# Kernel tuning notes

Hardware: AMD Instinct MI355X
Metric: run time of the kernel (lower is better)

## Reference

```python
import jax, jax.numpy as jnp
import numpy as np
import math

D_MODEL = 2048
N_HEADS = 16
D_K = D_MODEL // N_HEADS  # 128
B = 2
L = 2048


def _rope_cos_sin(seq_len, d_k, dtype):
    inv_freq = 1.0 / (10000.0 ** (jnp.arange(0, d_k, 2, dtype=jnp.float32) / d_k))
    t = jnp.arange(seq_len, dtype=jnp.float32)
    freqs = jnp.outer(t, inv_freq)  # [L, d_k//2]
    return jnp.cos(freqs).astype(dtype), jnp.sin(freqs).astype(dtype)


def _apply_rope(x, cos, sin):
    # x: [B, H, L, d_k]; cos/sin: [L, d_k//2] broadcast over B,H
    half = x.shape[-1] // 2
    x1, x2 = x[..., :half], x[..., half:]
    c = cos[None, None, :, :]
    s = sin[None, None, :, :]
    return jnp.concatenate([x1 * c - x2 * s, x1 * s + x2 * c], axis=-1)


def setup_inputs() -> dict:
    key = jax.random.key(0)
    ks = jax.random.split(key, 8)
    scale = 1.0 / math.sqrt(D_MODEL)
    query = jax.random.normal(ks[0], (B, L, D_MODEL), dtype=jnp.float32)
    k_in = jax.random.normal(ks[1], (B, L, D_MODEL), dtype=jnp.float32)
    v_in = jax.random.normal(ks[2], (B, L, D_MODEL), dtype=jnp.float32)
    w_q = jax.random.normal(ks[3], (D_MODEL, D_MODEL), dtype=jnp.float32) * scale
    w_k = jax.random.normal(ks[4], (D_MODEL, D_MODEL), dtype=jnp.float32) * scale
    w_v = jax.random.normal(ks[5], (D_MODEL, D_MODEL), dtype=jnp.float32) * scale
    w_o = jax.random.normal(ks[6], (D_MODEL, D_MODEL), dtype=jnp.float32) * scale
    mask = jnp.tril(jnp.ones((L, L), dtype=bool))[None, None, :, :]
    return {"query": query, "key": k_in, "value": v_in, "mask": mask,
            "w_q": w_q, "w_k": w_k, "w_v": w_v, "w_o": w_o}


def reference(query, key, value, mask, w_q, w_k, w_v, w_o):
    Bq, Lq, D = query.shape
    Lk = key.shape[1]
    # Linear (no bias): y = x @ W.T ; split heads -> [B, H, L, d_k]
    def proj(x, w, length):
        y = jnp.einsum('bld,ed->ble', x, w)
        return y.reshape(x.shape[0], length, N_HEADS, D_K).transpose(0, 2, 1, 3)
    Q = proj(query, w_q, Lq)
    K = proj(key, w_k, Lk)
    V = proj(value, w_v, Lk)
    cos_q, sin_q = _rope_cos_sin(Lq, D_K, query.dtype)
    cos_k, sin_k = _rope_cos_sin(Lk, D_K, key.dtype)
    Q = _apply_rope(Q, cos_q, sin_q)
    K = _apply_rope(K, cos_k, sin_k)
    scores = jnp.einsum('bhqd,bhkd->bhqk', Q, K) / math.sqrt(D_K)
    neg = jnp.finfo(scores.dtype).min
    scores = jnp.where(mask, scores, neg)
    attn = jax.nn.softmax(scores, axis=-1)
    out = jnp.einsum('bhqk,bhkd->bhqd', attn, V)
    out = out.transpose(0, 2, 1, 3).reshape(Bq, Lq, D)
    return jnp.einsum('bld,ed->ble', out, w_o)
```

## Files before the change

### kernel.cpp

```cpp
#include <hip/hip_runtime.h>
#include <stdint.h>

#define L_SEQ 2048
#define DMODEL 2048
#define NHEADS 16
#define DK 128
#define BATCH 2
#define MROWS (BATCH*L_SEQ)

typedef float f32x4 __attribute__((ext_vector_type(4)));
typedef short s16x8 __attribute__((ext_vector_type(8)));
typedef unsigned short u16;
typedef unsigned int u32;

__device__ __forceinline__ u16 f2bf(float f){
  u32 u = __builtin_bit_cast(u32, f);
  u += 0x7fffu + ((u >> 16) & 1u);
  return (u16)(u >> 16);
}
__device__ __forceinline__ float bf2f(u16 h){
  u32 u = ((u32)h) << 16;
  return __builtin_bit_cast(float, u);
}
__device__ __forceinline__ void gload_lds16(const void* g, void* l){
  __builtin_amdgcn_global_load_lds((const __attribute__((address_space(1))) void*)g,
                                   (__attribute__((address_space(3))) void*)l, 16, 0, 0);
}

__global__ void k_cvt_all(const float* __restrict__ s0, const float* __restrict__ s1,
                          const float* __restrict__ s2, const float* __restrict__ s3,
                          const float* __restrict__ s4, const float* __restrict__ s5,
                          const float* __restrict__ s6,
                          u16* __restrict__ d0, u16* __restrict__ d1, u16* __restrict__ d2,
                          u16* __restrict__ d3, u16* __restrict__ d4, u16* __restrict__ d5,
                          u16* __restrict__ d6){
  const int XC = MROWS*DMODEL/8;
  const int WC = DMODEL*DMODEL/8;
  const int total = 3*XC + 4*WC;
  int stride = gridDim.x * blockDim.x;
  for (int i = blockIdx.x*blockDim.x + threadIdx.x; i < total; i += stride){
    const float* s; u16* d; int j;
    if (i < XC)        { s=s0; d=d0; j=i; }
    else if (i < 2*XC) { s=s1; d=d1; j=i-XC; }
    else if (i < 3*XC) { s=s2; d=d2; j=i-2*XC; }
    else {
      int k2 = i - 3*XC; int wi = k2 / WC; j = k2 - wi*WC;
      s = wi==0?s3 : wi==1?s4 : wi==2?s5 : s6;
      d = wi==0?d3 : wi==1?d4 : wi==2?d5 : d6;
    }
    const f32x4* sp = (const f32x4*)s + (size_t)j*2;
    f32x4 a = sp[0], b = sp[1];
    s16x8 o;
    o[0]=(short)f2bf(a[0]); o[1]=(short)f2bf(a[1]); o[2]=(short)f2bf(a[2]); o[3]=(short)f2bf(a[3]);
    o[4]=(short)f2bf(b[0]); o[5]=(short)f2bf(b[1]); o[6]=(short)f2bf(b[2]); o[7]=(short)f2bf(b[3]);
    ((s16x8*)d)[j] = o;
  }
}

__global__ void k_tab(float* __restrict__ ct, float* __restrict__ st){
  int idx = blockIdx.x*blockDim.x + threadIdx.x;
  int l = idx >> 6, i = idx & 63;
  float e = (float)i * (1.0f/64.0f);
  float inv = 1.0f / powf(10000.0f, e);
  float fr = (float)l * inv;
  ct[idx] = cosf(fr);
  st[idx] = sinf(fr);
}

__global__ void k_rope2(u16* __restrict__ xq, u16* __restrict__ xk,
                        const float* __restrict__ ct, const float* __restrict__ st){
  int t0 = blockIdx.x*blockDim.x + threadIdx.x;
  u16* x = (t0 & (1<<19)) ? xk : xq;
  int t = t0 & ((1<<19)-1);
  int i8  = (t & 7) * 8;
  int h   = (t >> 3) & 15;
  int row = t >> 7;
  int l   = row & (L_SEQ-1);
  u16* p = x + (size_t)row*DMODEL + h*DK;
  s16x8 a  = *(s16x8*)(p + i8);
  s16x8 bq = *(s16x8*)(p + 64 + i8);
  const float* cp = ct + l*64 + i8;
  const float* sp = st + l*64 + i8;
  f32x4 c0 = *(const f32x4*)cp, c1 = *(const f32x4*)(cp+4);
  f32x4 s0 = *(const f32x4*)sp, s1 = *(const f32x4*)(sp+4);
  float cc[8] = {c0[0],c0[1],c0[2],c0[3],c1[0],c1[1],c1[2],c1[3]};
  float ss[8] = {s0[0],s0[1],s0[2],s0[3],s1[0],s1[1],s1[2],s1[3]};
  s16x8 y1, y2;
  #pragma unroll
  for (int e=0;e<8;e++){
    float x1 = bf2f((u16)a[e]), x2 = bf2f((u16)bq[e]);
    y1[e] = (short)f2bf(x1*cc[e] - x2*ss[e]);
    y2[e] = (short)f2bf(x1*ss[e] + x2*cc[e]);
  }
  *(s16x8*)(p + i8)      = y1;
  *(s16x8*)(p + 64 + i8) = y2;
}

__global__ __launch_bounds__(256)
void k_gemm3(const u16* __restrict__ A0, const u16* __restrict__ A1, const u16* __restrict__ A2,
             const u16* __restrict__ B0, const u16* __restrict__ B1, const u16* __restrict__ B2,
             u16* __restrict__ C0, u16* __restrict__ C1, u16* __restrict__ C2){
  __shared__ u16 As[128*64];
  __shared__ u16 Bs[128*64];
  const int z = blockIdx.z;
  const u16* __restrict__ A  = z==0?A0 : z==1?A1 : A2;
  const u16* __restrict__ Bw = z==0?B0 : z==1?B1 : B2;
  u16* __restrict__ Cb       = z==0?C0 : z==1?C1 : C2;
  const int tid = threadIdx.x, w = tid>>6, l = tid&63;
  const int lg = l>>4, lr = l&15;
  const int lin = (int)blockIdx.y*16 + (int)blockIdx.x;
  const int lin2 = (lin&7)*64 + (lin>>3);
  const int bm = (lin2>>4)*128, bn = (lin2&15)*128;
  const int K = DMODEL, N = DMODEL;
  f32x4 acc[4][4];
  #pragma unroll
  for (int i=0;i<4;i++)
    #pragma unroll
    for (int j=0;j<4;j++) acc[i][j] = (f32x4){0.f,0.f,0.f,0.f};

  const int chunkbase = w*64 + l;
  const int wm = (w>>1)*64, wn = (w&1)*64;

  for (int k0 = 0; k0 < K; k0 += 64){
    __syncthreads();
    #pragma unroll
    for (int i=0;i<4;i++){
      int chunk = i*256 + chunkbase;
      int row = chunk >> 3;
      int cbs = ((chunk&7)<<4) ^ ((row&7)<<4);
      const u16* ga = A  + (size_t)(bm+row)*K + k0 + (cbs>>1);
      const u16* gb = Bw + (size_t)(bn+row)*K + k0 + (cbs>>1);
      gload_lds16(ga, (void*)&As[(i*256 + w*64)*8]);
      gload_lds16(gb, (void*)&Bs[(i*256 + w*64)*8]);
    }
    __syncthreads();
    #pragma unroll
    for (int kc=0; kc<2; kc++){
      s16x8 af[4], bfr[4];
      #pragma unroll
      for (int mi=0; mi<4; mi++){
        int row = wm + mi*16 + lr;
        int off = row*128 + ((kc*64 + lg*16) ^ ((row&7)<<4));
        af[mi] = *(const s16x8*)((const char*)As + off);
      }
      #pragma unroll
      for (int ni=0; ni<4; ni++){
        int row = wn + ni*16 + lr;
        int off = row*128 + ((kc*64 + lg*16) ^ ((row&7)<<4));
        bfr[ni] = *(const s16x8*)((const char*)Bs + off);
      }
      #pragma unroll
      for (int mi=0; mi<4; mi++)
        #pragma unroll
        for (int ni=0; ni<4; ni++)
          acc[mi][ni] = __builtin_amdgcn_mfma_f32_16x16x32_bf16(af[mi], bfr[ni], acc[mi][ni], 0,0,0);
    }
  }
  #pragma unroll
  for (int mi=0; mi<4; mi++)
    #pragma unroll
    for (int ni=0; ni<4; ni++)
      #pragma unroll
      for (int r=0; r<4; r++){
        int row = bm + wm + mi*16 + (lg<<2) + r;
        int col = bn + wn + ni*16 + lr;
        Cb[(size_t)row*N + col] = f2bf(acc[mi][ni][r]);
      }
}

__global__ __launch_bounds__(256)
void k_gemm(const u16* __restrict__ A, const u16* __restrict__ Bw,
            float* __restrict__ Cf){
  __shared__ u16 As[128*64];
  __shared__ u16 Bs[128*64];
  const int tid = threadIdx.x, w = tid>>6, l = tid&63;
  const int lg = l>>4, lr = l&15;
  const int lin = (int)blockIdx.y*16 + (int)blockIdx.x;
  const int lin2 = (lin&7)*64 + (lin>>3);
  const int bm = (lin2>>4)*128, bn = (lin2&15)*128;
  const int K = DMODEL, N = DMODEL;
  f32x4 acc[4][4];
  #pragma unroll
  for (int i=0;i<4;i++)
    #pragma unroll
    for (int j=0;j<4;j++) acc[i][j] = (f32x4){0.f,0.f,0.f,0.f};

  const int chunkbase = w*64 + l;
  const int wm = (w>>1)*64, wn = (w&1)*64;

  for (int k0 = 0; k0 < K; k0 += 64){
    __syncthreads();
    #pragma unroll
    for (int i=0;i<4;i++){
      int chunk = i*256 + chunkbase;
      int row = chunk >> 3;
      int cbs = ((chunk&7)<<4) ^ ((row&7)<<4);
      const u16* ga = A  + (size_t)(bm+row)*K + k0 + (cbs>>1);
      const u16* gb = Bw + (size_t)(bn+row)*K + k0 + (cbs>>1);
      gload_lds16(ga, (void*)&As[(i*256 + w*64)*8]);
      gload_lds16(gb, (void*)&Bs[(i*256 + w*64)*8]);
    }
    __syncthreads();
    #pragma unroll
    for (int kc=0; kc<2; kc++){
      s16x8 af[4], bfr[4];
      #pragma unroll
      for (int mi=0; mi<4; mi++){
        int row = wm + mi*16 + lr;
        int off = row*128 + ((kc*64 + lg*16) ^ ((row&7)<<4));
        af[mi] = *(const s16x8*)((const char*)As + off);
      }
      #pragma unroll
      for (int ni=0; ni<4; ni++){
        int row = wn + ni*16 + lr;
        int off = row*128 + ((kc*64 + lg*16) ^ ((row&7)<<4));
        bfr[ni] = *(const s16x8*)((const char*)Bs + off);
      }
      #pragma unroll
      for (int mi=0; mi<4; mi++)
        #pragma unroll
        for (int ni=0; ni<4; ni++)
          acc[mi][ni] = __builtin_amdgcn_mfma_f32_16x16x32_bf16(af[mi], bfr[ni], acc[mi][ni], 0,0,0);
    }
  }
  #pragma unroll
  for (int mi=0; mi<4; mi++)
    #pragma unroll
    for (int ni=0; ni<4; ni++)
      #pragma unroll
      for (int r=0; r<4; r++){
        int row = bm + wm + mi*16 + (lg<<2) + r;
        int col = bn + wn + ni*16 + lr;
        Cf[(size_t)row*N + col] = acc[mi][ni][r];
      }
}

__global__ __launch_bounds__(256)
void k_attn(const u16* __restrict__ Qp, const u16* __restrict__ Kp,
            const u16* __restrict__ Vp, u16* __restrict__ AO){
  __shared__ u16 Ks[2][64*128];
  __shared__ u16 Vs[128*64];
  __shared__ u16 Ps[4][16*72];
  const int tid = threadIdx.x, w = tid>>6, l = tid&63;
  const int lg = l>>4, lr = l&15;
  const int lin = (int)blockIdx.y * (int)gridDim.x + (int)blockIdx.x;
  const int xcd = lin & 7, s8 = lin >> 3;
  const int bh  = xcd*4 + (s8 >> 4);
  const int qtp = s8 & 15;
  const int b = bh>>4, h = bh&15;
  const size_t kvbase = (size_t)(b*L_SEQ)*DMODEL + h*DK;
  const float scale = 0.08838834764831845f;

  u32 vv[2][8];
  s16x8 ones;
  #pragma unroll
  for (int e=0;e<8;e++) ones[e] = (short)0x3F80;

  auto issueK = [&](int j, int buf){
    #pragma unroll
    for (int i=0;i<4;i++){
      int chunk = i*256 + w*64 + l;
      int row = chunk >> 4;
      int cb = ((chunk&15)<<4) ^ ((row&7)<<4);
      const u16* src = Kp + kvbase + (size_t)(j*64 + row)*DMODEL + (cb>>1);
      gload_lds16(src, (void*)&Ks[buf][(i*256 + w*64)*8]);
    }
  };
  auto issueV = [&](int j){
    #pragma unroll
    for (int it=0; it<2; it++){
      int task = it*256 + tid;
      int dp = task & 63, kb = task >> 6;
      const u16* vsrc = Vp + kvbase + (size_t)(j*64 + kb*8)*DMODEL + dp*2;
      #pragma unroll
      for (int e=0;e<8;e++) vv[it][e] = *(const u32*)(vsrc + (size_t)e*DMODEL);
    }
  };
  auto writeV = [&](){
    #pragma unroll
    for (int it=0; it<2; it++){
      int task = it*256 + tid;
      int dp = task & 63, kb = task >> 6;
      int d0 = dp*2;
      s16x8 lo, hi;
      #pragma unroll
      for (int e=0;e<8;e++){ lo[e] = (short)(vv[it][e] & 0xffffu); hi[e] = (short)(vv[it][e] >> 16); }
      int g = ((d0>>1)&7)<<4;
      *(s16x8*)((char*)&Vs[0] + d0*128     + ((kb*16) ^ g)) = lo;
      *(s16x8*)((char*)&Vs[0] + (d0+1)*128 + ((kb*16) ^ g)) = hi;
    }
  };

  for (int half=0; half<2; half++){
    const int qt = half==0 ? qtp : 31-qtp;
    if (half) __syncthreads();

    s16x8 qf[4];
    {
      const u16* qptr = Qp + (size_t)(b*L_SEQ + qt*64 + w*16 + lr)*DMODEL + h*DK + lg*8;
      #pragma unroll
      for (int kc=0; kc<4; kc++) qf[kc] = *(const s16x8*)(qptr + kc*32);
    }
    f32x4 o[9];
    #pragma unroll
    for (int dt=0; dt<9; dt++) o[dt] = (f32x4){0.f,0.f,0.f,0.f};
    float mrow[4] = {-1e30f,-1e30f,-1e30f,-1e30f};

    issueK(0, 0);
    issueV(0);

    for (int j=0; j<=qt; j++){
      const int cur = j & 1;
      asm volatile("s_waitcnt vmcnt(16)" ::: "memory");
      __builtin_amdgcn_sched_barrier(0);
      __builtin_amdgcn_s_barrier();
      __builtin_amdgcn_sched_barrier(0);
      if (j < qt) issueK(j+1, cur^1);

      f32x4 st4[4];
      __builtin_amdgcn_s_setprio(1);
      #pragma unroll
      for (int ni=0; ni<4; ni++){
        f32x4 a = (f32x4){0.f,0.f,0.f,0.f};
        #pragma unroll
        for (int kc=0; kc<4; kc++){
          int row = ni*16 + lr;
          int off = row*256 + ((kc*64 + lg*16) ^ ((row&7)<<4));
          s16x8 kf = *(const s16x8*)((const char*)&Ks[cur][0] + off);
          a = __builtin_amdgcn_mfma_f32_16x16x32_bf16(qf[kc], kf, a, 0,0,0);
        }
        st4[ni] = a;
      }
      __builtin_amdgcn_s_setprio(0);

      float sv[4][4];
      float lanemax = -1e30f;
      const bool diag = (j == qt);
      #pragma unroll
      for (int r=0;r<4;r++){
        #pragma unroll
        for (int ni=0;ni<4;ni++){
          float x = st4[ni][r]*scale;
          if (diag){
            int kg = ni*16 + lr;
            int qg = w*16 + lg*4 + r;
            if (kg > qg) x = -1e30f;
          }
          sv[ni][r] = x;
          lanemax = fmaxf(lanemax, x);
        }
      }
      float mmin = fminf(fminf(mrow[0],mrow[1]), fminf(mrow[2],mrow[3]));
      if (!__all(lanemax <= mmin + 8.0f)){
        #pragma unroll
        for (int r=0;r<4;r++){
          float tm = fmaxf(fmaxf(sv[0][r],sv[1][r]), fmaxf(sv[2][r],sv[3][r]));
          #pragma unroll
          for (int msk=1; msk<16; msk<<=1) tm = fmaxf(tm, __shfl_xor(tm, msk, 64));
          float mn = fmaxf(mrow[r], tm);
          float al = __expf(mrow[r]-mn);
          mrow[r] = mn;
          #pragma unroll
          for (int dt=0;dt<9;dt++) o[dt][r] *= al;
        }
      }
      #pragma unroll
      for (int r=0;r<4;r++){
        #pragma unroll
        for (int ni=0;ni<4;ni++){
          float p = __expf(sv[ni][r]-mrow[r]);
          Ps[w][(lg*4 + r)*72 + ni*16 + lr] = f2bf(p);
        }
      }
      s16x8 pa[2];
      #pragma unroll
      for (int kc=0;kc<2;kc++) pa[kc] = *(const s16x8*)(&Ps[w][lr*72 + kc*32 + lg*8]);

      if (j < qt){ asm volatile("s_waitcnt vmcnt(4)" ::: "memory"); }
      else       { asm volatile("s_waitcnt vmcnt(0)" ::: "memory"); }
      __builtin_amdgcn_sched_barrier(0);
      writeV();
      if (j < qt) issueV(j+1);
      asm volatile("s_waitcnt lgkmcnt(0)" ::: "memory");
      __builtin_amdgcn_sched_barrier(0);
      __builtin_amdgcn_s_barrier();
      __builtin_amdgcn_sched_barrier(0);

      __builtin_amdgcn_s_setprio(1);
      #pragma unroll
      for (int dt=0;dt<8;dt++){
        #pragma unroll
        for (int kc=0;kc<2;kc++){
          int d = dt*16 + lr;
          int off = d*128 + ((kc*64 + lg*16) ^ (((d>>1)&7)<<4));
          s16x8 vf = *(const s16x8*)((const char*)&Vs[0] + off);
          o[dt] = __builtin_amdgcn_mfma_f32_16x16x32_bf16(pa[kc], vf, o[dt], 0,0,0);
        }
      }
      o[8] = __builtin_amdgcn_mfma_f32_16x16x32_bf16(pa[0], ones, o[8], 0,0,0);
      o[8] = __builtin_amdgcn_mfma_f32_16x16x32_bf16(pa[1], ones, o[8], 0,0,0);
      __builtin_amdgcn_s_setprio(0);
    }

    #pragma unroll
    for (int r=0;r<4;r++){
      float inv = 1.0f / o[8][r];
      size_t rowg = (size_t)(b*L_SEQ + qt*64 + w*16 + lg*4 + r);
      #pragma unroll
      for (int dt=0;dt<8;dt++)
        AO[rowg*DMODEL + h*DK + dt*16 + lr] = f2bf(o[dt][r]*inv);
    }
  }
}

extern "C" void kernel_launch(void* const* d_in, const int* in_sizes, int n_in,
                              void* d_out, int out_size, void* d_ws, size_t ws_size,
                              hipStream_t stream){
  const float* q  = (const float*)d_in[0];
  const float* k  = (const float*)d_in[1];
  const float* v  = (const float*)d_in[2];
  const float* wq = (const float*)d_in[4];
  const float* wk = (const float*)d_in[5];
  const float* wv = (const float*)d_in[6];
  const float* wo = (const float*)d_in[7];
  (void)in_sizes; (void)n_in; (void)out_size; (void)ws_size;

  const size_t MD = (size_t)MROWS*DMODEL;
  const size_t DD = (size_t)DMODEL*DMODEL;
  char* ws = (char*)d_ws;
  size_t off = 0;
  auto alloc = [&](size_t bytes)->void*{ void* p = ws + off; off += (bytes + 255) & ~(size_t)255; return p; };
  u16* Xq = (u16*)alloc(MD*2);
  u16* Xk = (u16*)alloc(MD*2);
  u16* Xv = (u16*)alloc(MD*2);
  u16* Wq = (u16*)alloc(DD*2);
  u16* Wk = (u16*)alloc(DD*2);
  u16* Wv = (u16*)alloc(DD*2);
  u16* Wo = (u16*)alloc(DD*2);
  u16* Qp = (u16*)alloc(MD*2);
  u16* Kp = (u16*)alloc(MD*2);
  u16* Vp = (u16*)alloc(MD*2);
  float* ct = (float*)alloc((size_t)L_SEQ*64*4);
  float* st = (float*)alloc((size_t)L_SEQ*64*4);
  u16* AO = Xq;

  k_cvt_all<<<2048,256,0,stream>>>(q, k, v, wq, wk, wv, wo,
                                   Xq, Xk, Xv, Wq, Wk, Wv, Wo);
  k_tab<<<512,256,0,stream>>>(ct, st);

  k_gemm3<<<dim3(16,32,3),256,0,stream>>>(Xq, Xk, Xv, Wq, Wk, Wv, Qp, Kp, Vp);
  k_rope2<<<4096,256,0,stream>>>(Qp, Kp, ct, st);
  k_attn<<<dim3(16,32),256,0,stream>>>(Qp, Kp, Vp, AO);
  k_gemm<<<dim3(16,32),256,0,stream>>>(AO, Wo, (float*)d_out);
}
```

Before: 275.0 us.

## Double-buffer GEMM LDS tiles with 256x128 blocks of 512 threads

Both projection GEMM kernels switch to 256x128 output tiles computed by 8 waves, with double-buffered LDS. The next K-tile's global-to-LDS loads are issued before the current tile's MFMAs, using explicit vmcnt waits and barriers, and MFMA sections get raised wave priority. This aims to hide global load latency behind compute and reuse the B tile across a taller M tile, at the cost of more LDS (96KB per block) and fewer blocks in flight.

New measurement: 301.7 us. 1.1x slower.

```diff
diff --git a/kernel.cpp b/kernel.cpp
--- a/kernel.cpp
+++ b/kernel.cpp
@@ -96,12 +96,12 @@
   *(s16x8*)(p + 64 + i8) = y2;
 }
 
-__global__ __launch_bounds__(256)
+__global__ __launch_bounds__(512)
 void k_gemm3(const u16* __restrict__ A0, const u16* __restrict__ A1, const u16* __restrict__ A2,
              const u16* __restrict__ B0, const u16* __restrict__ B1, const u16* __restrict__ B2,
              u16* __restrict__ C0, u16* __restrict__ C1, u16* __restrict__ C2){
-  __shared__ u16 As[128*64];
-  __shared__ u16 Bs[128*64];
+  __shared__ u16 As[2][256*64];
+  __shared__ u16 Bs[2][128*64];
   const int z = blockIdx.z;
   const u16* __restrict__ A  = z==0?A0 : z==1?A1 : A2;
   const u16* __restrict__ Bw = z==0?B0 : z==1?B1 : B2;
@@ -109,31 +109,46 @@
   const int tid = threadIdx.x, w = tid>>6, l = tid&63;
   const int lg = l>>4, lr = l&15;
   const int lin = (int)blockIdx.y*16 + (int)blockIdx.x;
-  const int lin2 = (lin&7)*64 + (lin>>3);
-  const int bm = (lin2>>4)*128, bn = (lin2&15)*128;
+  const int lin2 = (lin&7)*32 + (lin>>3);
+  const int bm = (lin2>>4)*256, bn = (lin2&15)*128;
   const int K = DMODEL, N = DMODEL;
+  const int wm = (w>>1)*64, wn = (w&1)*64;
   f32x4 acc[4][4];
   #pragma unroll
   for (int i=0;i<4;i++)
     #pragma unroll
     for (int j=0;j<4;j++) acc[i][j] = (f32x4){0.f,0.f,0.f,0.f};
 
-  const int chunkbase = w*64 + l;
-  const int wm = (w>>1)*64, wn = (w&1)*64;
-
-  for (int k0 = 0; k0 < K; k0 += 64){
-    __syncthreads();
+  auto stage = [&](int t, int buf){
+    const int k0 = t*64;
     #pragma unroll
     for (int i=0;i<4;i++){
-      int chunk = i*256 + chunkbase;
+      int chunk = i*512 + tid;
       int row = chunk >> 3;
       int cbs = ((chunk&7)<<4) ^ ((row&7)<<4);
-      const u16* ga = A  + (size_t)(bm+row)*K + k0 + (cbs>>1);
-      const u16* gb = Bw + (size_t)(bn+row)*K + k0 + (cbs>>1);
-      gload_lds16(ga, (void*)&As[(i*256 + w*64)*8]);
-      gload_lds16(gb, (void*)&Bs[(i*256 + w*64)*8]);
-    }
-    __syncthreads();
+      gload_lds16(A + (size_t)(bm+row)*K + k0 + (cbs>>1), (void*)&As[buf][chunk*8]);
+    }
+    #pragma unroll
+    for (int i=0;i<2;i++){
+      int chunk = i*512 + tid;
+      int row = chunk >> 3;
+      int cbs = ((chunk&7)<<4) ^ ((row&7)<<4);
+      gload_lds16(Bw + (size_t)(bn+row)*K + k0 + (cbs>>1), (void*)&Bs[buf][chunk*8]);
+    }
+  };
+
+  stage(0, 0);
+  const int nk = K/64;
+  for (int t=0; t<nk; t++){
+    const int cur = t&1;
+    __builtin_amdgcn_s_barrier();
+    __builtin_amdgcn_sched_barrier(0);
+    if (t+1 < nk) stage(t+1, cur^1);
+    if (t+1 < nk){ asm volatile("s_waitcnt vmcnt(6)" ::: "memory"); }
+    else         { asm volatile("s_waitcnt vmcnt(0)" ::: "memory"); }
+    __builtin_amdgcn_sched_barrier(0);
+    __builtin_amdgcn_s_barrier();
+    __builtin_amdgcn_sched_barrier(0);
     #pragma unroll
     for (int kc=0; kc<2; kc++){
       s16x8 af[4], bfr[4];
@@ -141,19 +156,21 @@
       for (int mi=0; mi<4; mi++){
         int row = wm + mi*16 + lr;
         int off = row*128 + ((kc*64 + lg*16) ^ ((row&7)<<4));
-        af[mi] = *(const s16x8*)((const char*)As + off);
+        af[mi] = *(const s16x8*)((const char*)&As[cur][0] + off);
       }
       #pragma unroll
       for (int ni=0; ni<4; ni++){
         int row = wn + ni*16 + lr;
         int off = row*128 + ((kc*64 + lg*16) ^ ((row&7)<<4));
-        bfr[ni] = *(const s16x8*)((const char*)Bs + off);
-      }
+        bfr[ni] = *(const s16x8*)((const char*)&Bs[cur][0] + off);
+      }
+      __builtin_amdgcn_s_setprio(1);
       #pragma unroll
       for (int mi=0; mi<4; mi++)
         #pragma unroll
         for (int ni=0; ni<4; ni++)
           acc[mi][ni] = __builtin_amdgcn_mfma_f32_16x16x32_bf16(af[mi], bfr[ni], acc[mi][ni], 0,0,0);
+      __builtin_amdgcn_s_setprio(0);
     }
   }
   #pragma unroll
@@ -168,39 +185,54 @@
       }
 }
 
-__global__ __launch_bounds__(256)
+__global__ __launch_bounds__(512)
 void k_gemm(const u16* __restrict__ A, const u16* __restrict__ Bw,
             float* __restrict__ Cf){
-  __shared__ u16 As[128*64];
-  __shared__ u16 Bs[128*64];
+  __shared__ u16 As[2][256*64];
+  __shared__ u16 Bs[2][128*64];
   const int tid = threadIdx.x, w = tid>>6, l = tid&63;
   const int lg = l>>4, lr = l&15;
   const int lin = (int)blockIdx.y*16 + (int)blockIdx.x;
-  const int lin2 = (lin&7)*64 + (lin>>3);
-  const int bm = (lin2>>4)*128, bn = (lin2&15)*128;
+  const int lin2 = (lin&7)*32 + (lin>>3);
+  const int bm = (lin2>>4)*256, bn = (lin2&15)*128;
   const int K = DMODEL, N = DMODEL;
+  const int wm = (w>>1)*64, wn = (w&1)*64;
   f32x4 acc[4][4];
   #pragma unroll
   for (int i=0;i<4;i++)
     #pragma unroll
     for (int j=0;j<4;j++) acc[i][j] = (f32x4){0.f,0.f,0.f,0.f};
 
-  const int chunkbase = w*64 + l;
-  const int wm = (w>>1)*64, wn = (w&1)*64;
-
-  for (int k0 = 0; k0 < K; k0 += 64){
-    __syncthreads();
+  auto stage = [&](int t, int buf){
+    const int k0 = t*64;
     #pragma unroll
     for (int i=0;i<4;i++){
-      int chunk = i*256 + chunkbase;
+      int chunk = i*512 + tid;
       int row = chunk >> 3;
       int cbs = ((chunk&7)<<4) ^ ((row&7)<<4);
-      const u16* ga = A  + (size_t)(bm+row)*K + k0 + (cbs>>1);
-      const u16* gb = Bw + (size_t)(bn+row)*K + k0 + (cbs>>1);
-      gload_lds16(ga, (void*)&As[(i*256 + w*64)*8]);
-      gload_lds16(gb, (void*)&Bs[(i*256 + w*64)*8]);
-    }
-    __syncthreads();
+      gload_lds16(A + (size_t)(bm+row)*K + k0 + (cbs>>1), (void*)&As[buf][chunk*8]);
+    }
+    #pragma unroll
+    for (int i=0;i<2;i++){
+      int chunk = i*512 + tid;
+      int row = chunk >> 3;
+      int cbs = ((chunk&7)<<4) ^ ((row&7)<<4);
+      gload_lds16(Bw + (size_t)(bn+row)*K + k0 + (cbs>>1), (void*)&Bs[buf][chunk*8]);
+    }
+  };
+
+  stage(0, 0);
+  const int nk = K/64;
+  for (int t=0; t<nk; t++){
+    const int cur = t&1;
+    __builtin_amdgcn_s_barrier();
+    __builtin_amdgcn_sched_barrier(0);
+    if (t+1 < nk) stage(t+1, cur^1);
+    if (t+1 < nk){ asm volatile("s_waitcnt vmcnt(6)" ::: "memory"); }
+    else         { asm volatile("s_waitcnt vmcnt(0)" ::: "memory"); }
+    __builtin_amdgcn_sched_barrier(0);
+    __builtin_amdgcn_s_barrier();
+    __builtin_amdgcn_sched_barrier(0);
     #pragma unroll
     for (int kc=0; kc<2; kc++){
       s16x8 af[4], bfr[4];
@@ -208,19 +240,21 @@
       for (int mi=0; mi<4; mi++){
         int row = wm + mi*16 + lr;
         int off = row*128 + ((kc*64 + lg*16) ^ ((row&7)<<4));
-        af[mi] = *(const s16x8*)((const char*)As + off);
+        af[mi] = *(const s16x8*)((const char*)&As[cur][0] + off);
       }
       #pragma unroll
       for (int ni=0; ni<4; ni++){
         int row = wn + ni*16 + lr;
         int off = row*128 + ((kc*64 + lg*16) ^ ((row&7)<<4));
-        bfr[ni] = *(const s16x8*)((const char*)Bs + off);
-      }
+        bfr[ni] = *(const s16x8*)((const char*)&Bs[cur][0] + off);
+      }
+      __builtin_amdgcn_s_setprio(1);
       #pragma unroll
       for (int mi=0; mi<4; mi++)
         #pragma unroll
         for (int ni=0; ni<4; ni++)
           acc[mi][ni] = __builtin_amdgcn_mfma_f32_16x16x32_bf16(af[mi], bfr[ni], acc[mi][ni], 0,0,0);
+      __builtin_amdgcn_s_setprio(0);
     }
   }
   #pragma unroll
@@ -448,8 +482,8 @@
                                    Xq, Xk, Xv, Wq, Wk, Wv, Wo);
   k_tab<<<512,256,0,stream>>>(ct, st);
 
-  k_gemm3<<<dim3(16,32,3),256,0,stream>>>(Xq, Xk, Xv, Wq, Wk, Wv, Qp, Kp, Vp);
+  k_gemm3<<<dim3(16,16,3),512,0,stream>>>(Xq, Xk, Xv, Wq, Wk, Wv, Qp, Kp, Vp);
   k_rope2<<<4096,256,0,stream>>>(Qp, Kp, ct, st);
   k_attn<<<dim3(16,32),256,0,stream>>>(Qp, Kp, Vp, AO);
-  k_gemm<<<dim3(16,32),256,0,stream>>>(AO, Wo, (float*)d_out);
-}
+  k_gemm<<<dim3(16,16),512,0,stream>>>(AO, Wo, (float*)d_out);
+}
```
